# Optimization experiments

Hardware: AMD Instinct MI355X
Metric: run time of the kernel (lower is better)

Reference implementation:

```python
import jax, jax.numpy as jnp
import numpy as np


def setup_inputs() -> dict:
    key = jax.random.key(0)
    k1, k2, k3, k4, k5 = jax.random.split(key, 5)
    b, n, L, D, m = 8, 8192, 512, 128, 16
    x = jax.random.normal(k1, (b, n, L), dtype=jnp.float32)
    # attention MLP: Linear(L->D, no bias), Tanh, Linear(D->1, no bias)
    W1 = jax.random.normal(k2, (L, D), dtype=jnp.float32) / np.sqrt(L).astype(np.float32)
    W2 = jax.random.normal(k3, (D, 1), dtype=jnp.float32) / np.sqrt(D).astype(np.float32)
    batched_image_ids = jax.random.randint(k4, (b, n), 0, m)  # which image each packed token belongs to
    key_pad_mask = jax.random.bernoulli(k5, 0.1, (b, n))      # True = padding token
    return {"x": x, "W1": W1, "W2": W2,
            "batched_image_ids": batched_image_ids,
            "key_pad_mask": key_pad_mask,
            "max_queries": 16}


def reference(x, W1, W2, batched_image_ids, key_pad_mask, max_queries):
    # Attention scores per token: tanh(x W1) W2 -> [b, n, 1]
    A = jnp.tanh(x @ W1) @ W2
    A = jnp.swapaxes(A, -1, -2)  # [b, 1, n]
    b, n, d = x.shape
    # Per-image pooling mask: token j contributes to query i iff its image id == i and not padded
    image_id_arange = jnp.arange(max_queries)                                    # [m]
    attn_pool_mask = (image_id_arange[None, :, None] == batched_image_ids[:, None, :])
    attn_pool_mask = attn_pool_mask & (~key_pad_mask)[:, None, :]                # [b, m, n]
    neg = -jnp.finfo(A.dtype).max
    A = jnp.where(attn_pool_mask, jnp.broadcast_to(A, (b, max_queries, n)), neg)
    A = jax.nn.softmax(A, axis=-1)                                               # [b, m, n]
    out = jnp.einsum('bmn,bnd->bmd', A, x)                                       # pooled per image
    # num_images == max_queries for every bag -> is_images selects everything
    out = out.reshape(b * max_queries, d)
    return out
```

## Files before the change

kernel.cpp:

```cpp
#include <hip/hip_runtime.h>
#include <hip/hip_bf16.h>
#include <cstdint>
#include <cstddef>

typedef __attribute__((ext_vector_type(8))) short bf16x8;
typedef __attribute__((ext_vector_type(4))) float f32x4;

#define BATCH 8
#define NTOK 8192
#define LDIM 512
#define DDIM 128
#define NQ 16
#define NSEG 8
#define SEGLEN (NTOK / NSEG)

static __device__ __forceinline__ short f2bf(float f) {
  uint32_t u = __float_as_uint(f);
  uint32_t r = u + 0x7fffu + ((u >> 16) & 1u);
  return (short)(r >> 16);
}

static __device__ __forceinline__ bf16x8 cvt8(float4 a, float4 b) {
  bf16x8 o;
  o[0] = f2bf(a.x); o[1] = f2bf(a.y); o[2] = f2bf(a.z); o[3] = f2bf(a.w);
  o[4] = f2bf(b.x); o[5] = f2bf(b.y); o[6] = f2bf(b.z); o[7] = f2bf(b.w);
  return o;
}

static __device__ __forceinline__ bool is_pad(const void* pad, int byteFlag, int j) {
  return byteFlag ? (((const unsigned char*)pad)[j] != 0)
                  : (((const int*)pad)[j] != 0);
}

__global__ __launch_bounds__(256) void k0_wfrag(const float* __restrict__ W1,
                                                short* __restrict__ wfrag,
                                                const unsigned int* __restrict__ pad_raw,
                                                int* __restrict__ flag) {
  int tid = blockIdx.x * blockDim.x + threadIdx.x;
  if (tid < 16 * 8 * 64) {
    int l = tid & 63;
    int t = (tid >> 6) & 7;
    int c = tid >> 9;
    int kbase = c * 32 + (l >> 4) * 8;
    int col = t * 16 + (l & 15);
    bf16x8 frag;
#pragma unroll
    for (int i = 0; i < 8; ++i) frag[i] = f2bf(W1[(size_t)(kbase + i) * DDIM + col]);
    ((bf16x8*)wfrag)[tid] = frag;
  }
  if (blockIdx.x == 0) {
    int any_gt1 = 0;
    for (int i = threadIdx.x; i < 16384; i += 256)
      if (pad_raw[i] > 1u) any_gt1 = 1;
    unsigned long long m = __ballot(any_gt1);
    __shared__ int s[4];
    if ((threadIdx.x & 63) == 0) s[threadIdx.x >> 6] = (m != 0ull) ? 1 : 0;
    __syncthreads();
    if (threadIdx.x == 0) flag[0] = (s[0] | s[1] | s[2] | s[3]);
  }
}

__global__ __launch_bounds__(512, 6) void k1_scores(const float* __restrict__ x,
                                                    const short* __restrict__ wfrag,
                                                    const float* __restrict__ W2,
                                                    float* __restrict__ expw) {
  __shared__ short ldsw[16384];
  const int tid = threadIdx.x, wave = tid >> 6, lane = tid & 63;
  const int rowBase = blockIdx.x * 128 + wave * 16;
  const float* xp = x + (size_t)(rowBase + (lane & 15)) * LDIM + ((lane >> 4) * 8);

#define STAGE(qd)                                                                             \
  {                                                                                           \
    const unsigned int* src_ = (const unsigned int*)wfrag + (qd) * 8192;                      \
    _Pragma("unroll")                                                                         \
    for (int i = 0; i < 4; ++i) {                                                             \
      __builtin_amdgcn_global_load_lds(                                                       \
          (const __attribute__((address_space(1))) unsigned int*)(src_ + (i * 512 + tid) * 4),\
          (__attribute__((address_space(3))) unsigned int*)&ldsw[(i * 512 + wave * 64) * 8],  \
          16, 0, 0);                                                                          \
    }                                                                                         \
  }

#define ALOAD(dst, c)                                  \
  {                                                    \
    dst[0] = *(const float4*)(xp + (c) * 32);          \
    dst[1] = *(const float4*)(xp + (c) * 32 + 4);      \
  }

  f32x4 acc[8];
#pragma unroll
  for (int t = 0; t < 8; ++t) acc[t] = (f32x4){0.f, 0.f, 0.f, 0.f};
  float4 avbuf[4][2];

  STAGE(0);
  ALOAD(avbuf[0], 0);
  ALOAD(avbuf[1], 1);
  ALOAD(avbuf[2], 2);
  ALOAD(avbuf[3], 3);
  __syncthreads();

#pragma unroll
  for (int qd = 0; qd < 4; ++qd) {
#pragma unroll
    for (int cc = 0; cc < 4; ++cc) {
      const int c = qd * 4 + cc;
      bf16x8 af = cvt8(avbuf[c & 3][0], avbuf[c & 3][1]);
      if (c < 12) ALOAD(avbuf[c & 3], c + 4);
#pragma unroll
      for (int t = 0; t < 8; ++t) {
        bf16x8 bfr = *(const bf16x8*)&ldsw[((cc * 8 + t) * 64 + lane) * 8];
        acc[t] = __builtin_amdgcn_mfma_f32_16x16x32_bf16(af, bfr, acc[t], 0, 0, 0);
      }
    }
    if (qd < 3) {
      __syncthreads();
      STAGE(qd + 1);
      __syncthreads();
    }
  }
#undef STAGE
#undef ALOAD

  float w2v[8];
#pragma unroll
  for (int t = 0; t < 8; ++t) w2v[t] = W2[t * 16 + (lane & 15)];
  float asum[4] = {0.f, 0.f, 0.f, 0.f};
#pragma unroll
  for (int t = 0; t < 8; ++t) {
#pragma unroll
    for (int r = 0; r < 4; ++r) {
      float h = 1.f - 2.f / (__expf(2.f * acc[t][r]) + 1.f);
      asum[r] += h * w2v[t];
    }
  }
#pragma unroll
  for (int m = 1; m < 16; m <<= 1) {
#pragma unroll
    for (int r = 0; r < 4; ++r) asum[r] += __shfl_xor(asum[r], m, 64);
  }
  if ((lane & 15) == 0) {
    int rb = rowBase + (lane >> 4) * 4;
#pragma unroll
    for (int r = 0; r < 4; ++r) expw[rb + r] = __expf(asum[r]);
  }
}

__global__ __launch_bounds__(512) void k3_pool(const float* __restrict__ x,
                                               const float* __restrict__ expw,
                                               const int* __restrict__ ids,
                                               const void* __restrict__ pad,
                                               const int* __restrict__ flag,
                                               float* __restrict__ partial,
                                               float* __restrict__ wsum) {
  int blk = blockIdx.x;
  int s = blk & 7, q = (blk >> 3) & 15, b = blk >> 7;
  int wave = threadIdx.x >> 6, lane = threadIdx.x & 63;
  int bfl = flag[0];
  __shared__ float w_u[1024];
  __shared__ unsigned short j_u[1024];
  __shared__ int cnt[8];
  __shared__ float wred[8];

  const int base = b * NTOK;
  const int tokBase = s * SEGLEN + wave * 128;

  int myCnt = 0;
#pragma unroll
  for (int g = 0; g < 2; ++g) {
    int j = tokBase + g * 64 + lane;
    bool mem = (ids[base + j] == q) && !is_pad(pad, bfl, base + j);
    myCnt += __popcll(__ballot(mem));
  }
  if (lane == 0) cnt[wave] = myCnt;
  __syncthreads();

  int wpos = 0;
#pragma unroll
  for (int w = 0; w < 8; ++w) if (w < wave) wpos += cnt[w];
  const int total = cnt[0] + cnt[1] + cnt[2] + cnt[3] + cnt[4] + cnt[5] + cnt[6] + cnt[7];

  float wacc = 0.f;
#pragma unroll
  for (int g = 0; g < 2; ++g) {
    int j = tokBase + g * 64 + lane;
    bool mem = (ids[base + j] == q) && !is_pad(pad, bfl, base + j);
    float wt = mem ? expw[base + j] : 0.f;
    wacc += wt;
    unsigned long long mask = __ballot(mem);
    if (mem) {
      int pos = wpos + __popcll(mask & ((1ull << lane) - 1ull));
      w_u[pos] = wt;
      j_u[pos] = (unsigned short)j;
    }
    wpos += __popcll(mask);
  }
#pragma unroll
  for (int m = 1; m < 64; m <<= 1) wacc += __shfl_xor(wacc, m, 64);
  if (lane == 0) wred[wave] = wacc;
  __syncthreads();

  int grp = threadIdx.x >> 7, ct = threadIdx.x & 127;
  int c0 = ct * 4;
  int per = (total + 3) >> 2;
  int e0 = grp * per;
  int e1 = e0 + per; if (e1 > total) e1 = total;
  float4 av = {0.f, 0.f, 0.f, 0.f};
  if (e0 < e1) {
    float4 cur = *(const float4*)(x + (size_t)(base + j_u[e0]) * LDIM + c0);
    int e = e0;
    for (; e + 1 < e1; ++e) {
      float4 nxt = *(const float4*)(x + (size_t)(base + j_u[e + 1]) * LDIM + c0);
      float wt = w_u[e];
      av.x = fmaf(wt, cur.x, av.x); av.y = fmaf(wt, cur.y, av.y);
      av.z = fmaf(wt, cur.z, av.z); av.w = fmaf(wt, cur.w, av.w);
      cur = nxt;
    }
    float wt = w_u[e];
    av.x = fmaf(wt, cur.x, av.x); av.y = fmaf(wt, cur.y, av.y);
    av.z = fmaf(wt, cur.z, av.z); av.w = fmaf(wt, cur.w, av.w);
  }
  *(float4*)(partial + ((size_t)(blk * 4 + grp)) * LDIM + c0) = av;
  if (threadIdx.x == 0)
    wsum[blk] = wred[0] + wred[1] + wred[2] + wred[3] + wred[4] + wred[5] + wred[6] + wred[7];
}

__global__ __launch_bounds__(512) void k4_reduce(const float* __restrict__ partial,
                                                 const float* __restrict__ wsum,
                                                 float* __restrict__ out) {
  int bq = blockIdx.x;
  int b = bq >> 4, q = bq & 15;
  int c = threadIdx.x;
  float ws = 0.f;
#pragma unroll
  for (int s = 0; s < 8; ++s) ws += wsum[b * 128 + q * 8 + s];
  float ps = 0.f;
#pragma unroll
  for (int s = 0; s < 8; ++s)
#pragma unroll
    for (int g = 0; g < 4; ++g)
      ps += partial[((size_t)((b * 128 + q * 8 + s) * 4 + g)) * LDIM + c];
  out[bq * 512 + c] = (ws > 0.f) ? (ps / ws) : 0.f;
}

extern "C" void kernel_launch(void* const* d_in, const int* in_sizes, int n_in,
                              void* d_out, int out_size, void* d_ws, size_t ws_size,
                              hipStream_t stream) {
  const float* x = (const float*)d_in[0];
  const float* W1 = (const float*)d_in[1];
  const float* W2 = (const float*)d_in[2];
  const int* ids = (const int*)d_in[3];
  const void* pad = d_in[4];
  float* out = (float*)d_out;

  char* ws = (char*)d_ws;
  short* wfrag = (short*)ws;
  int* flag = (int*)(ws + 131072);
  float* expw = (float*)(ws + 131200);
  float* wsum = (float*)(ws + 393344);
  float* partial = (float*)(ws + 397440);

  hipLaunchKernelGGL(k0_wfrag, dim3(32), dim3(256), 0, stream,
                     W1, wfrag, (const unsigned int*)pad, flag);
  hipLaunchKernelGGL(k1_scores, dim3((BATCH * NTOK) / 128), dim3(512), 0, stream,
                     x, wfrag, W2, expw);
  hipLaunchKernelGGL(k3_pool, dim3(BATCH * NQ * NSEG), dim3(512), 0, stream,
                     x, expw, ids, pad, flag, partial, wsum);
  hipLaunchKernelGGL(k4_reduce, dim3(BATCH * NQ), dim3(512), 0, stream,
                     partial, wsum, out);
}
```

Baseline: 66.58 us.

## Deepen x prefetch, use packed bf16 convert, and load membership once in pooling

The scores kernel now converts fp32 to bf16 with the hardware packed convert instruction instead of manual rounding. It also prefetches six x chunks ahead instead of four, and lowers the occupancy hint from 6 to 4 waves so the extra registers fit. The pooling kernel reads ids, pad and expw once and keeps the ballots, where before it ran two passes over the same tokens. Deeper prefetch hides more global latency but cuts occupancy. The hardware convert may round differently in edge cases.

```diff
diff --git a/kernel.cpp b/kernel.cpp
--- a/kernel.cpp
+++ b/kernel.cpp
@@ -21,10 +21,12 @@
 }
 
 static __device__ __forceinline__ bf16x8 cvt8(float4 a, float4 b) {
-  bf16x8 o;
-  o[0] = f2bf(a.x); o[1] = f2bf(a.y); o[2] = f2bf(a.z); o[3] = f2bf(a.w);
-  o[4] = f2bf(b.x); o[5] = f2bf(b.y); o[6] = f2bf(b.z); o[7] = f2bf(b.w);
-  return o;
+  union { uint32_t u[4]; bf16x8 v; } r;
+  asm("v_cvt_pk_bf16_f32 %0, %1, %2" : "=v"(r.u[0]) : "v"(a.x), "v"(a.y));
+  asm("v_cvt_pk_bf16_f32 %0, %1, %2" : "=v"(r.u[1]) : "v"(a.z), "v"(a.w));
+  asm("v_cvt_pk_bf16_f32 %0, %1, %2" : "=v"(r.u[2]) : "v"(b.x), "v"(b.y));
+  asm("v_cvt_pk_bf16_f32 %0, %1, %2" : "=v"(r.u[3]) : "v"(b.z), "v"(b.w));
+  return r.v;
 }
 
 static __device__ __forceinline__ bool is_pad(const void* pad, int byteFlag, int j) {
@@ -60,7 +62,7 @@
   }
 }
 
-__global__ __launch_bounds__(512, 6) void k1_scores(const float* __restrict__ x,
+__global__ __launch_bounds__(512, 4) void k1_scores(const float* __restrict__ x,
                                                     const short* __restrict__ wfrag,
                                                     const float* __restrict__ W2,
                                                     float* __restrict__ expw) {
@@ -90,13 +92,15 @@
   f32x4 acc[8];
 #pragma unroll
   for (int t = 0; t < 8; ++t) acc[t] = (f32x4){0.f, 0.f, 0.f, 0.f};
-  float4 avbuf[4][2];
+  float4 avbuf[6][2];
 
   STAGE(0);
   ALOAD(avbuf[0], 0);
   ALOAD(avbuf[1], 1);
   ALOAD(avbuf[2], 2);
   ALOAD(avbuf[3], 3);
+  ALOAD(avbuf[4], 4);
+  ALOAD(avbuf[5], 5);
   __syncthreads();
 
 #pragma unroll
@@ -104,8 +108,8 @@
 #pragma unroll
     for (int cc = 0; cc < 4; ++cc) {
       const int c = qd * 4 + cc;
-      bf16x8 af = cvt8(avbuf[c & 3][0], avbuf[c & 3][1]);
-      if (c < 12) ALOAD(avbuf[c & 3], c + 4);
+      bf16x8 af = cvt8(avbuf[c % 6][0], avbuf[c % 6][1]);
+      if (c < 10) ALOAD(avbuf[c % 6], c + 6);
 #pragma unroll
       for (int t = 0; t < 8; ++t) {
         bf16x8 bfr = *(const bf16x8*)&ldsw[((cc * 8 + t) * 64 + lane) * 8];
@@ -164,14 +168,14 @@
   const int base = b * NTOK;
   const int tokBase = s * SEGLEN + wave * 128;
 
-  int myCnt = 0;
-#pragma unroll
-  for (int g = 0; g < 2; ++g) {
-    int j = tokBase + g * 64 + lane;
-    bool mem = (ids[base + j] == q) && !is_pad(pad, bfl, base + j);
-    myCnt += __popcll(__ballot(mem));
-  }
-  if (lane == 0) cnt[wave] = myCnt;
+  int j0 = tokBase + lane, j1 = tokBase + 64 + lane;
+  bool mem0 = (ids[base + j0] == q) && !is_pad(pad, bfl, base + j0);
+  bool mem1 = (ids[base + j1] == q) && !is_pad(pad, bfl, base + j1);
+  float wt0 = mem0 ? expw[base + j0] : 0.f;
+  float wt1 = mem1 ? expw[base + j1] : 0.f;
+  unsigned long long m0 = __ballot(mem0), m1 = __ballot(mem1);
+  int c0w = __popcll(m0), c1w = __popcll(m1);
+  if (lane == 0) cnt[wave] = c0w + c1w;
   __syncthreads();
 
   int wpos = 0;
@@ -179,21 +183,16 @@
   for (int w = 0; w < 8; ++w) if (w < wave) wpos += cnt[w];
   const int total = cnt[0] + cnt[1] + cnt[2] + cnt[3] + cnt[4] + cnt[5] + cnt[6] + cnt[7];
 
-  float wacc = 0.f;
-#pragma unroll
-  for (int g = 0; g < 2; ++g) {
-    int j = tokBase + g * 64 + lane;
-    bool mem = (ids[base + j] == q) && !is_pad(pad, bfl, base + j);
-    float wt = mem ? expw[base + j] : 0.f;
-    wacc += wt;
-    unsigned long long mask = __ballot(mem);
-    if (mem) {
-      int pos = wpos + __popcll(mask & ((1ull << lane) - 1ull));
-      w_u[pos] = wt;
-      j_u[pos] = (unsigned short)j;
-    }
-    wpos += __popcll(mask);
-  }
+  unsigned long long below = (1ull << lane) - 1ull;
+  if (mem0) {
+    int pos = wpos + __popcll(m0 & below);
+    w_u[pos] = wt0; j_u[pos] = (unsigned short)j0;
+  }
+  if (mem1) {
+    int pos = wpos + c0w + __popcll(m1 & below);
+    w_u[pos] = wt1; j_u[pos] = (unsigned short)j1;
+  }
+  float wacc = wt0 + wt1;
 #pragma unroll
   for (int m = 1; m < 64; m <<= 1) wacc += __shfl_xor(wacc, m, 64);
   if (lane == 0) wred[wave] = wacc;
```

After: 67.25 us. Within noise of the previous version (+1.0%).
